# Performance work log

Hardware: AMD Instinct MI355X
Metric: run time of the kernel (lower is better)

Reference implementation:

```python
import jax, jax.numpy as jnp
import numpy as np

K = 5        # kernel_size
F0 = 3       # features[0]
F1 = 3       # features[1]
N = 2097152  # ring length (number of sites)
NOISE = 0.01

# triple_product[a,b,c] = cross(tetra[a], tetra[b]) @ tetra[c], shape (4,4,4)
_t = np.array([[0.0, 0.0, 1.0],
               [(8/9)**0.5, 0.0, -1/3],
               [-(2/9)**0.5, (2/3)**0.5, -1/3],
               [-(2/9)**0.5, -(2/3)**0.5, -1/3]], dtype=np.float64)
_cross = np.cross(_t[:, None, :], _t[None, :, :])          # (4,4,3)
TRIPLE_PRODUCT = jnp.asarray(np.einsum('abd,cd->abc', _cross, _t), dtype=jnp.float32)


def setup_inputs() -> dict:
    key = jax.random.key(0)
    ks = jax.random.split(key, 5)
    x = jax.random.randint(ks[0], (N,), 0, 4, dtype=jnp.int32)
    input_kernel_dot = NOISE * jax.random.normal(ks[1], (F0, K), jnp.float32)
    input_kernel_triple = NOISE * jax.random.normal(ks[2], (F0, K, K), jnp.float32)
    kernel_0 = jax.random.normal(ks[3], (K, 2 * F0, F1), jnp.float32) / np.float32(np.sqrt(K * 2 * F0))
    bias_0 = jnp.zeros((1, F1), jnp.float32)
    dense_w = jax.random.normal(ks[4], (F1, 1), jnp.float32) / np.float32(np.sqrt(F1))
    return {"x": x, "input_kernel_dot": input_kernel_dot,
            "input_kernel_triple": input_kernel_triple, "kernel_0": kernel_0,
            "bias_0": bias_0, "dense_w": dense_w}


def reference(x, input_kernel_dot, input_kernel_triple, kernel_0, bias_0, dense_w):
    n = x.shape[0]
    i = jnp.arange(n)
    # ring neighbors x[(i+1)..(i+K) mod N], shape (N, K)
    nbr = (i[:, None] + jnp.arange(1, K + 1)[None, :]) % n
    xn = x[nbr]
    # dot channel: +/-1 same-spin indicator contracted with (F0,K) kernel
    same = 2.0 * (x[:, None] == xn).astype(jnp.float32) - 1.0      # (N,K)
    y_dot = jnp.einsum('fk,nk->nf', input_kernel_dot, same)        # (N,F0)
    # triple channel: antisymmetrized kernel against triple-product lookup
    anti = input_kernel_triple - jnp.swapaxes(input_kernel_triple, 1, 2)   # (F0,K,K)
    tpl = TRIPLE_PRODUCT[x[:, None, None], xn[:, :, None], xn[:, None, :]]  # (N,K,K)
    y_triple = jnp.einsum('fjk,njk->nf', anti, tpl)                # (N,F0)
    y = jax.nn.elu(jnp.concatenate([y_dot, y_triple], axis=1))     # (N,2*F0)
    # circular conv layer: roll(y, i)[:K][j] == y[(j - i) % N]
    conv_idx = (jnp.arange(K)[None, :] - i[:, None]) % n           # (N,K)
    y = jnp.einsum('jcf,njc->nf', kernel_0, y[conv_idx]) + bias_0  # (N,F1)
    y = jax.nn.elu(y)
    y = jnp.mean(y, axis=0)                                        # (F1,)
    return (y @ dense_w).ravel()[0]
```

## Files before the change

kernel.cpp:

```cpp
#include <hip/hip_runtime.h>
#include <math.h>

#define NSITES 2097152
#define NMASK  (NSITES - 1)

__device__ __forceinline__ float elu1(float v) {
    return v > 0.0f ? v : __expf(v) - 1.0f;
}

__device__ __forceinline__ float tp_val(int a, int b, int c) {
    if (a == b || b == c || a == c) return 0.0f;
    int inv = (a > b) + (a > c) + (b > c);
    int d   = 6 - a - b - c;
    float base = (d & 1) ? 0.76980035891950105f : -0.76980035891950105f;
    return (inv & 1) ? -base : base;
}

__global__ __launch_bounds__(256) void build_tables(
    const float* __restrict__ kdot,
    const float* __restrict__ ktri,
    float*       __restrict__ ws)
{
    float4* tab4 = reinterpret_cast<float4*>(ws);
    float2* tab2 = reinterpret_cast<float2*>(ws + 16384);

    const int code = blockIdx.x * 256 + threadIdx.x;
    const int a = code & 3;
    int nb[5];
    #pragma unroll
    for (int k = 0; k < 5; ++k) nb[k] = (code >> (2 + 2 * k)) & 3;

    float yd0 = 0.f, yd1 = 0.f, yd2 = 0.f;
    #pragma unroll
    for (int k = 0; k < 5; ++k) {
        const float sm = (a == nb[k]) ? 1.0f : -1.0f;
        yd0 = fmaf(kdot[0 * 5 + k], sm, yd0);
        yd1 = fmaf(kdot[1 * 5 + k], sm, yd1);
        yd2 = fmaf(kdot[2 * 5 + k], sm, yd2);
    }

    float yt0 = 0.f, yt1 = 0.f, yt2 = 0.f;
    #pragma unroll
    for (int j = 0; j < 5; ++j)
        #pragma unroll
        for (int k = j + 1; k < 5; ++k) {
            const float t = tp_val(a, nb[j], nb[k]);
            const float a0 = 2.0f * (ktri[0 * 25 + j * 5 + k] - ktri[0 * 25 + k * 5 + j]);
            const float a1 = 2.0f * (ktri[1 * 25 + j * 5 + k] - ktri[1 * 25 + k * 5 + j]);
            const float a2 = 2.0f * (ktri[2 * 25 + j * 5 + k] - ktri[2 * 25 + k * 5 + j]);
            yt0 = fmaf(a0, t, yt0);
            yt1 = fmaf(a1, t, yt1);
            yt2 = fmaf(a2, t, yt2);
        }

    tab4[code] = make_float4(elu1(yd0), elu1(yd1), elu1(yd2), elu1(yt0));
    tab2[code] = make_float2(elu1(yt1), elu1(yt2));
}

__global__ __launch_bounds__(1024) void conv_kernel(
    const int*   __restrict__ x,
    const float* __restrict__ k0,
    const float* __restrict__ bias,
    const float* __restrict__ dw,
    const float* __restrict__ ws,
    float*       __restrict__ out)
{
    __shared__ float4 s4[4096];
    __shared__ float2 s2[4096];
    __shared__ float  red[16];

    const int tid = threadIdx.x;

    {
        const float4* tab4 = reinterpret_cast<const float4*>(ws);
        const float2* tab2 = reinterpret_cast<const float2*>(ws + 16384);
        #pragma unroll
        for (int i = 0; i < 4; ++i) {
            const int idx = tid + 1024 * i;
            s4[idx] = tab4[idx];
            s2[idx] = tab2[idx];
        }
    }
    __syncthreads();

    const int m0 = (blockIdx.x * 1024 + tid) * 8;
    int xv[20];
    #pragma unroll
    for (int c = 0; c < 5; ++c) {
        const int4 v = *reinterpret_cast<const int4*>(x + ((m0 + 4 * c) & NMASK));
        xv[4 * c + 0] = v.x; xv[4 * c + 1] = v.y;
        xv[4 * c + 2] = v.z; xv[4 * c + 3] = v.w;
    }

    unsigned long long code = 0ull;
    #pragma unroll
    for (int j = 0; j < 17; ++j)
        code |= (unsigned long long)(unsigned)xv[j] << (2 * j);

    const float b0 = bias[0], b1 = bias[1], b2 = bias[2];
    float acc[8][3];
    #pragma unroll
    for (int o = 0; o < 8; ++o) { acc[o][0] = b0; acc[o][1] = b1; acc[o][2] = b2; }

    #pragma unroll
    for (int i = 0; i < 12; ++i) {
        const int idx = (int)((code >> (2 * i)) & 0xFFFull);
        const float4 a4 = s4[idx];
        const float2 a2 = s2[idx];
        const float y[6] = { a4.x, a4.y, a4.z, a4.w, a2.x, a2.y };
        #pragma unroll
        for (int j = 0; j < 5; ++j) {
            const int o = i - j;
            if (o >= 0 && o < 8) {
                #pragma unroll
                for (int c = 0; c < 6; ++c) {
                    const int kb = (j * 6 + c) * 3;
                    acc[o][0] = fmaf(k0[kb + 0], y[c], acc[o][0]);
                    acc[o][1] = fmaf(k0[kb + 1], y[c], acc[o][1]);
                    acc[o][2] = fmaf(k0[kb + 2], y[c], acc[o][2]);
                }
            }
        }
    }

    const float d0 = dw[0], d1 = dw[1], d2 = dw[2];
    float partial = 0.0f;
    #pragma unroll
    for (int o = 0; o < 8; ++o)
        partial += elu1(acc[o][0]) * d0 + elu1(acc[o][1]) * d1 + elu1(acc[o][2]) * d2;

    #pragma unroll
    for (int off = 32; off > 0; off >>= 1)
        partial += __shfl_down(partial, off, 64);

    if ((tid & 63) == 0) red[tid >> 6] = partial;
    __syncthreads();

    if (tid == 0) {
        float s = 0.0f;
        #pragma unroll
        for (int w = 0; w < 16; ++w) s += red[w];
        atomicAdd(out, s * (1.0f / (float)NSITES));
    }
}

extern "C" void kernel_launch(void* const* d_in, const int* in_sizes, int n_in,
                              void* d_out, int out_size, void* d_ws, size_t ws_size,
                              hipStream_t stream) {
    const int*   x    = (const int*)  d_in[0];
    const float* kdot = (const float*)d_in[1];
    const float* ktri = (const float*)d_in[2];
    const float* k0   = (const float*)d_in[3];
    const float* bias = (const float*)d_in[4];
    const float* dw   = (const float*)d_in[5];
    float* out = (float*)d_out;
    float* ws  = (float*)d_ws;

    hipMemsetAsync(out, 0, sizeof(float), stream);
    build_tables<<<16, 256, 0, stream>>>(kdot, ktri, ws);
    conv_kernel<<<NSITES / 8192, 1024, 0, stream>>>(x, k0, bias, dw, ws, out);
}
```

Measured before the change: 87.12 us.

## Fuse table build into conv kernel and prefetch x before table construction

```diff
diff --git a/kernel.cpp b/kernel.cpp
--- a/kernel.cpp
+++ b/kernel.cpp
@@ -16,82 +16,93 @@
     return (inv & 1) ? -base : base;
 }
 
-__global__ __launch_bounds__(256) void build_tables(
+__global__ __launch_bounds__(1024) void su2_fused_kernel(
+    const int*   __restrict__ x,
     const float* __restrict__ kdot,
     const float* __restrict__ ktri,
-    float*       __restrict__ ws)
-{
-    float4* tab4 = reinterpret_cast<float4*>(ws);
-    float2* tab2 = reinterpret_cast<float2*>(ws + 16384);
-
-    const int code = blockIdx.x * 256 + threadIdx.x;
-    const int a = code & 3;
-    int nb[5];
-    #pragma unroll
-    for (int k = 0; k < 5; ++k) nb[k] = (code >> (2 + 2 * k)) & 3;
-
-    float yd0 = 0.f, yd1 = 0.f, yd2 = 0.f;
-    #pragma unroll
-    for (int k = 0; k < 5; ++k) {
-        const float sm = (a == nb[k]) ? 1.0f : -1.0f;
-        yd0 = fmaf(kdot[0 * 5 + k], sm, yd0);
-        yd1 = fmaf(kdot[1 * 5 + k], sm, yd1);
-        yd2 = fmaf(kdot[2 * 5 + k], sm, yd2);
-    }
-
-    float yt0 = 0.f, yt1 = 0.f, yt2 = 0.f;
-    #pragma unroll
-    for (int j = 0; j < 5; ++j)
-        #pragma unroll
-        for (int k = j + 1; k < 5; ++k) {
-            const float t = tp_val(a, nb[j], nb[k]);
-            const float a0 = 2.0f * (ktri[0 * 25 + j * 5 + k] - ktri[0 * 25 + k * 5 + j]);
-            const float a1 = 2.0f * (ktri[1 * 25 + j * 5 + k] - ktri[1 * 25 + k * 5 + j]);
-            const float a2 = 2.0f * (ktri[2 * 25 + j * 5 + k] - ktri[2 * 25 + k * 5 + j]);
-            yt0 = fmaf(a0, t, yt0);
-            yt1 = fmaf(a1, t, yt1);
-            yt2 = fmaf(a2, t, yt2);
-        }
-
-    tab4[code] = make_float4(elu1(yd0), elu1(yd1), elu1(yd2), elu1(yt0));
-    tab2[code] = make_float2(elu1(yt1), elu1(yt2));
-}
-
-__global__ __launch_bounds__(1024) void conv_kernel(
-    const int*   __restrict__ x,
     const float* __restrict__ k0,
     const float* __restrict__ bias,
     const float* __restrict__ dw,
-    const float* __restrict__ ws,
     float*       __restrict__ out)
 {
     __shared__ float4 s4[4096];
     __shared__ float2 s2[4096];
+    __shared__ float  tp[64];
     __shared__ float  red[16];
 
     const int tid = threadIdx.x;
 
-    {
-        const float4* tab4 = reinterpret_cast<const float4*>(ws);
-        const float2* tab2 = reinterpret_cast<const float2*>(ws + 16384);
+    const int m0 = (blockIdx.x * 1024 + tid) * 8;
+    int4 xraw[5];
+    #pragma unroll
+    for (int c = 0; c < 5; ++c)
+        xraw[c] = *reinterpret_cast<const int4*>(x + ((m0 + 4 * c) & NMASK));
+
+    if (tid < 64) tp[tid] = tp_val(tid >> 4, (tid >> 2) & 3, tid & 3);
+
+    float kd[3][5];
+    #pragma unroll
+    for (int f = 0; f < 3; ++f)
         #pragma unroll
-        for (int i = 0; i < 4; ++i) {
-            const int idx = tid + 1024 * i;
-            s4[idx] = tab4[idx];
-            s2[idx] = tab2[idx];
-        }
+        for (int k = 0; k < 5; ++k) kd[f][k] = kdot[f * 5 + k];
+
+    float an[3][10];
+    #pragma unroll
+    for (int f = 0; f < 3; ++f) {
+        int p = 0;
+        #pragma unroll
+        for (int j = 0; j < 5; ++j)
+            #pragma unroll
+            for (int k = j + 1; k < 5; ++k) {
+                an[f][p] = 2.0f * (ktri[f * 25 + j * 5 + k] - ktri[f * 25 + k * 5 + j]);
+                ++p;
+            }
     }
     __syncthreads();
 
-    const int m0 = (blockIdx.x * 1024 + tid) * 8;
+    #pragma unroll
+    for (int i = 0; i < 4; ++i) {
+        const int code = tid + 1024 * i;
+        const int a = code & 3;
+        int nb[5];
+        #pragma unroll
+        for (int k = 0; k < 5; ++k) nb[k] = (code >> (2 + 2 * k)) & 3;
+
+        float yd0 = 0.f, yd1 = 0.f, yd2 = 0.f;
+        #pragma unroll
+        for (int k = 0; k < 5; ++k) {
+            const float sm = (a == nb[k]) ? 1.0f : -1.0f;
+            yd0 = fmaf(kd[0][k], sm, yd0);
+            yd1 = fmaf(kd[1][k], sm, yd1);
+            yd2 = fmaf(kd[2][k], sm, yd2);
+        }
+
+        float yt0 = 0.f, yt1 = 0.f, yt2 = 0.f;
+        {
+            int p = 0;
+            #pragma unroll
+            for (int j = 0; j < 5; ++j)
+                #pragma unroll
+                for (int k = j + 1; k < 5; ++k) {
+                    const float t = tp[(a << 4) + (nb[j] << 2) + nb[k]];
+                    yt0 = fmaf(an[0][p], t, yt0);
+                    yt1 = fmaf(an[1][p], t, yt1);
+                    yt2 = fmaf(an[2][p], t, yt2);
+                    ++p;
+                }
+        }
+
+        s4[code] = make_float4(elu1(yd0), elu1(yd1), elu1(yd2), elu1(yt0));
+        s2[code] = make_float2(elu1(yt1), elu1(yt2));
+    }
+    __syncthreads();
+
     int xv[20];
     #pragma unroll
     for (int c = 0; c < 5; ++c) {
-        const int4 v = *reinterpret_cast<const int4*>(x + ((m0 + 4 * c) & NMASK));
-        xv[4 * c + 0] = v.x; xv[4 * c + 1] = v.y;
-        xv[4 * c + 2] = v.z; xv[4 * c + 3] = v.w;
+        xv[4 * c + 0] = xraw[c].x; xv[4 * c + 1] = xraw[c].y;
+        xv[4 * c + 2] = xraw[c].z; xv[4 * c + 3] = xraw[c].w;
     }
-
     unsigned long long code = 0ull;
     #pragma unroll
     for (int j = 0; j < 17; ++j)
@@ -154,9 +165,7 @@
     const float* bias = (const float*)d_in[4];
     const float* dw   = (const float*)d_in[5];
     float* out = (float*)d_out;
-    float* ws  = (float*)d_ws;
 
     hipMemsetAsync(out, 0, sizeof(float), stream);
-    build_tables<<<16, 256, 0, stream>>>(kdot, ktri, ws);
-    conv_kernel<<<NSITES / 8192, 1024, 0, stream>>>(x, k0, bias, dw, ws, out);
+    su2_fused_kernel<<<NSITES / 8192, 1024, 0, stream>>>(x, kdot, ktri, k0, bias, dw, out);
 }
```

Result: faster. 84.80 us (-2.7%).
